# Kernel optimization log

Measured on AMD Instinct MI355X. Metric: run time of the kernel, lower is better.

## Reference

```python
import jax, jax.numpy as jnp
import numpy as np

WIN = 7          # gaussian window size (odd)
SIGMA = 1.5
DOWNSCALE = 2
C1 = 0.01 ** 2
C2 = 0.03 ** 2


def _gauss_window(dtype):
    x = jnp.arange(WIN, dtype=jnp.float32) - (WIN - 1) / 2
    g = jnp.exp(-x ** 2 / (2 * SIGMA ** 2))
    g = g / g.sum()
    w2d = jnp.outer(g, g)                      # (7,7)
    return w2d[None, None].astype(dtype)       # OIHW = (1,1,7,7)


def _avg_pool(x, k):
    if k == 1:
        return x
    s = jax.lax.reduce_window(x, 0.0, jax.lax.add,
                              (1, 1, k, k), (1, 1, k, k), 'VALID')
    return s / (k * k)


def _blur(x, w):
    pad = WIN // 2
    return jax.lax.conv_general_dilated(
        x, w, window_strides=(1, 1),
        padding=[(pad, pad), (pad, pad)],
        dimension_numbers=('NCHW', 'OIHW', 'NCHW'))


def setup_inputs() -> dict:
    key = jax.random.key(0)
    k1, k2 = jax.random.split(key)
    shape = (16, 1, 768, 1024)
    pred = jax.random.uniform(k1, shape, dtype=jnp.float32)
    target = jax.random.uniform(k2, shape, dtype=jnp.float32)
    return {"pred": pred, "target": target}


def reference(pred, target):
    p = _avg_pool(pred, DOWNSCALE)
    t = _avg_pool(target, DOWNSCALE)
    w = _gauss_window(p.dtype)

    mu1 = _blur(p, w)
    mu2 = _blur(t, w)
    mu1_sq = mu1 * mu1
    mu2_sq = mu2 * mu2
    mu1_mu2 = mu1 * mu2

    sigma1_sq = _blur(p * p, w) - mu1_sq
    sigma2_sq = _blur(t * t, w) - mu2_sq
    sigma12 = _blur(p * t, w) - mu1_mu2

    num = (2 * mu1_mu2 + C1) * (2 * sigma12 + C2)
    den = (mu1_sq + mu2_sq + C1) * (sigma1_sq + sigma2_sq + C2)
    ssim_map = num / (den + 1e-12)
    return 1.0 - ssim_map.mean()
```

## Files before the change

kernel.cpp:

```cpp
#include <hip/hip_runtime.h>
#include <math.h>

#define NIMG 16
#define IH 768
#define IW 1024
#define HD 384
#define WD 512
#define TH 16
#define TW 64
#define HALO 3
#define RH (TH + 2*HALO)
#define RW (TW + 2*HALO)
#define RWP 72
#define NGX (WD/TW)
#define NGY (HD/TH)
#define NBLK (NGX*NGY*NIMG)
#define SSIM_C1 1.0e-4f
#define SSIM_C2 9.0e-4f

struct GW { float g[7]; };

__global__ __launch_bounds__(256, 4) void ssim_main(
    const float* __restrict__ pred, const float* __restrict__ tgt,
    float* __restrict__ partial, GW gw)
{
  __shared__ float p_s[RH][RWP];
  __shared__ float t_s[RH][RWP];
  __shared__ float vb[5][TH][RWP];
  __shared__ float wred[4];

  const int tid = threadIdx.x;
  const int bx = blockIdx.x, by = blockIdx.y, n = blockIdx.z;
  const int tx0 = bx * TW, ty0 = by * TH;
  const float* __restrict__ pb = pred + (size_t)n * IH * IW;
  const float* __restrict__ tb = tgt  + (size_t)n * IH * IW;

  for (int idx = tid; idx < RH * RW; idx += 256) {
    const int ly = idx / RW;
    const int lx = idx - ly * RW;
    const int gy = ty0 + ly - HALO;
    const int gx = tx0 + lx - HALO;
    float pv = 0.f, tv = 0.f;
    if ((unsigned)gy < (unsigned)HD && (unsigned)gx < (unsigned)WD) {
      const size_t o0 = (size_t)(2 * gy) * IW + (size_t)(2 * gx);
      const float2 a = *(const float2*)(pb + o0);
      const float2 b = *(const float2*)(pb + o0 + IW);
      const float2 c = *(const float2*)(tb + o0);
      const float2 d = *(const float2*)(tb + o0 + IW);
      pv = 0.25f * ((a.x + a.y) + (b.x + b.y));
      tv = 0.25f * ((c.x + c.y) + (d.x + d.y));
    }
    p_s[ly][lx] = pv;
    t_s[ly][lx] = tv;
  }
  __syncthreads();

  for (int idx = tid; idx < TH * (RWP/4); idx += 256) {
    const int y  = idx / (RWP/4);
    const int c4 = (idx - y * (RWP/4)) * 4;
    float m1_0=0,m1_1=0,m1_2=0,m1_3=0;
    float m2_0=0,m2_1=0,m2_2=0,m2_3=0;
    float pp_0=0,pp_1=0,pp_2=0,pp_3=0;
    float tt_0=0,tt_1=0,tt_2=0,tt_3=0;
    float pt_0=0,pt_1=0,pt_2=0,pt_3=0;
#pragma unroll
    for (int k = 0; k < 7; ++k) {
      const float w = gw.g[k];
      const float4 P = *(const float4*)&p_s[y + k][c4];
      const float4 T = *(const float4*)&t_s[y + k][c4];
      m1_0 += w*P.x;        m1_1 += w*P.y;        m1_2 += w*P.z;        m1_3 += w*P.w;
      m2_0 += w*T.x;        m2_1 += w*T.y;        m2_2 += w*T.z;        m2_3 += w*T.w;
      pp_0 += w*(P.x*P.x);  pp_1 += w*(P.y*P.y);  pp_2 += w*(P.z*P.z);  pp_3 += w*(P.w*P.w);
      tt_0 += w*(T.x*T.x);  tt_1 += w*(T.y*T.y);  tt_2 += w*(T.z*T.z);  tt_3 += w*(T.w*T.w);
      pt_0 += w*(P.x*T.x);  pt_1 += w*(P.y*T.y);  pt_2 += w*(P.z*T.z);  pt_3 += w*(P.w*T.w);
    }
    *(float4*)&vb[0][y][c4] = make_float4(m1_0, m1_1, m1_2, m1_3);
    *(float4*)&vb[1][y][c4] = make_float4(m2_0, m2_1, m2_2, m2_3);
    *(float4*)&vb[2][y][c4] = make_float4(pp_0, pp_1, pp_2, pp_3);
    *(float4*)&vb[3][y][c4] = make_float4(tt_0, tt_1, tt_2, tt_3);
    *(float4*)&vb[4][y][c4] = make_float4(pt_0, pt_1, pt_2, pt_3);
  }
  __syncthreads();

  float lsum = 0.f;
  for (int idx = tid; idx < TH * (TW/4); idx += 256) {
    const int y  = idx / (TW/4);
    const int c0 = (idx - y * (TW/4)) * 4;
    float w0[12], w1[12], w2[12], w3[12], w4[12];
#define LDCH(arr, ch) { \
      const float4 A = *(const float4*)&vb[ch][y][c0];     \
      const float4 B = *(const float4*)&vb[ch][y][c0 + 4]; \
      const float4 C = *(const float4*)&vb[ch][y][c0 + 8]; \
      arr[0]=A.x; arr[1]=A.y; arr[2]=A.z;  arr[3]=A.w;     \
      arr[4]=B.x; arr[5]=B.y; arr[6]=B.z;  arr[7]=B.w;     \
      arr[8]=C.x; arr[9]=C.y; arr[10]=C.z; arr[11]=C.w; }
    LDCH(w0, 0) LDCH(w1, 1) LDCH(w2, 2) LDCH(w3, 3) LDCH(w4, 4)
#undef LDCH
#pragma unroll
    for (int j = 0; j < 4; ++j) {
      float mu1 = 0.f, mu2 = 0.f, bpp = 0.f, btt = 0.f, bpt = 0.f;
#pragma unroll
      for (int k = 0; k < 7; ++k) {
        const float w = gw.g[k];
        mu1 += w * w0[j + k];
        mu2 += w * w1[j + k];
        bpp += w * w2[j + k];
        btt += w * w3[j + k];
        bpt += w * w4[j + k];
      }
      const float mu1sq = mu1 * mu1;
      const float mu2sq = mu2 * mu2;
      const float mu12  = mu1 * mu2;
      const float s1    = bpp - mu1sq;
      const float s2    = btt - mu2sq;
      const float s12   = bpt - mu12;
      const float num = (2.f * mu12 + SSIM_C1) * (2.f * s12 + SSIM_C2);
      const float den = (mu1sq + mu2sq + SSIM_C1) * (s1 + s2 + SSIM_C2);
      lsum += num / (den + 1e-12f);
    }
  }

#pragma unroll
  for (int off = 32; off > 0; off >>= 1)
    lsum += __shfl_down(lsum, off, 64);
  if ((tid & 63) == 0) wred[tid >> 6] = lsum;
  __syncthreads();
  if (tid == 0)
    partial[((size_t)n * NGY + by) * NGX + bx] =
        wred[0] + wred[1] + wred[2] + wred[3];
}

__global__ __launch_bounds__(256) void ssim_final(
    const float* __restrict__ partial, float* __restrict__ out)
{
  __shared__ float red[4];
  float s = 0.f;
  for (int i = threadIdx.x; i < NBLK; i += 256) s += partial[i];
#pragma unroll
  for (int off = 32; off > 0; off >>= 1)
    s += __shfl_down(s, off, 64);
  if ((threadIdx.x & 63) == 0) red[threadIdx.x >> 6] = s;
  __syncthreads();
  if (threadIdx.x == 0) {
    const float tot = red[0] + red[1] + red[2] + red[3];
    out[0] = 1.0f - tot * (1.0f / (float)((size_t)NIMG * HD * WD));
  }
}

extern "C" void kernel_launch(void* const* d_in, const int* in_sizes, int n_in,
                              void* d_out, int out_size, void* d_ws, size_t ws_size,
                              hipStream_t stream) {
  const float* pred = (const float*)d_in[0];
  const float* tgt  = (const float*)d_in[1];
  float* out     = (float*)d_out;
  float* partial = (float*)d_ws;

  GW gw;
  double gd[7], s = 0.0;
  for (int i = 0; i < 7; ++i) {
    const double x = (double)i - 3.0;
    gd[i] = exp(-x * x / (2.0 * 1.5 * 1.5));
    s += gd[i];
  }
  for (int i = 0; i < 7; ++i) gw.g[i] = (float)(gd[i] / s);

  dim3 grid(NGX, NGY, NIMG);
  ssim_main<<<grid, 256, 0, stream>>>(pred, tgt, partial, gw);
  ssim_final<<<1, 256, 0, stream>>>(partial, out);
}
```

Baseline: 139.8 us.

## Fuse vertical and horizontal blur passes in registers, vectorize halo loads

Removes the shared-memory intermediate buffer holding the five vertical-blur channels and its barrier. Each thread now computes vertical sums for 12 columns in registers and then applies the horizontal blur directly. The horizontal halo widens to 4 so global loads can be float4, with two downsampled pixels per slot. Occupancy hint is raised to 5 waves. The cost is about three times more vertical-blur arithmetic per thread, because neighbouring threads recompute overlapping columns, plus higher register pressure.

```diff
diff --git a/kernel.cpp b/kernel.cpp
--- a/kernel.cpp
+++ b/kernel.cpp
@@ -8,10 +8,12 @@
 #define WD 512
 #define TH 16
 #define TW 64
-#define HALO 3
-#define RH (TH + 2*HALO)
-#define RW (TW + 2*HALO)
-#define RWP 72
+#define HALO_Y 3
+#define HALO_X 4
+#define RH (TH + 2*HALO_Y)
+#define RW (TW + 2*HALO_X)
+#define NPAIR (RW/2)
+#define NSLOT (RH*NPAIR)
 #define NGX (WD/TW)
 #define NGY (HD/TH)
 #define NBLK (NGX*NGY*NIMG)
@@ -20,13 +22,12 @@
 
 struct GW { float g[7]; };
 
-__global__ __launch_bounds__(256, 4) void ssim_main(
+__global__ __launch_bounds__(256, 5) void ssim_main(
     const float* __restrict__ pred, const float* __restrict__ tgt,
     float* __restrict__ partial, GW gw)
 {
-  __shared__ float p_s[RH][RWP];
-  __shared__ float t_s[RH][RWP];
-  __shared__ float vb[5][TH][RWP];
+  __shared__ float p_s[RH][RW];
+  __shared__ float t_s[RH][RW];
   __shared__ float wred[4];
 
   const int tid = threadIdx.x;
@@ -35,89 +36,83 @@
   const float* __restrict__ pb = pred + (size_t)n * IH * IW;
   const float* __restrict__ tb = tgt  + (size_t)n * IH * IW;
 
-  for (int idx = tid; idx < RH * RW; idx += 256) {
-    const int ly = idx / RW;
-    const int lx = idx - ly * RW;
-    const int gy = ty0 + ly - HALO;
-    const int gx = tx0 + lx - HALO;
-    float pv = 0.f, tv = 0.f;
-    if ((unsigned)gy < (unsigned)HD && (unsigned)gx < (unsigned)WD) {
-      const size_t o0 = (size_t)(2 * gy) * IW + (size_t)(2 * gx);
-      const float2 a = *(const float2*)(pb + o0);
-      const float2 b = *(const float2*)(pb + o0 + IW);
-      const float2 c = *(const float2*)(tb + o0);
-      const float2 d = *(const float2*)(tb + o0 + IW);
-      pv = 0.25f * ((a.x + a.y) + (b.x + b.y));
-      tv = 0.25f * ((c.x + c.y) + (d.x + d.y));
+#pragma unroll
+  for (int i = 0; i < 4; ++i) {
+    const int slot = tid + i * 256;
+    if (slot < NSLOT) {
+      const int row  = slot / NPAIR;
+      const int pair = slot - row * NPAIR;
+      const int gy = ty0 + row - HALO_Y;
+      const int pg = tx0 + 2 * pair - HALO_X;
+      float pv0 = 0.f, pv1 = 0.f, tv0 = 0.f, tv1 = 0.f;
+      if ((unsigned)gy < (unsigned)HD && (unsigned)pg < (unsigned)WD) {
+        const size_t o0 = (size_t)(2 * gy) * IW + (size_t)(2 * pg);
+        const float4 a = *(const float4*)(pb + o0);
+        const float4 b = *(const float4*)(pb + o0 + IW);
+        const float4 c = *(const float4*)(tb + o0);
+        const float4 d = *(const float4*)(tb + o0 + IW);
+        pv0 = 0.25f * ((a.x + a.y) + (b.x + b.y));
+        pv1 = 0.25f * ((a.z + a.w) + (b.z + b.w));
+        tv0 = 0.25f * ((c.x + c.y) + (d.x + d.y));
+        tv1 = 0.25f * ((c.z + c.w) + (d.z + d.w));
+      }
+      *(float2*)&p_s[row][2 * pair] = make_float2(pv0, pv1);
+      *(float2*)&t_s[row][2 * pair] = make_float2(tv0, tv1);
     }
-    p_s[ly][lx] = pv;
-    t_s[ly][lx] = tv;
   }
   __syncthreads();
 
-  for (int idx = tid; idx < TH * (RWP/4); idx += 256) {
-    const int y  = idx / (RWP/4);
-    const int c4 = (idx - y * (RWP/4)) * 4;
-    float m1_0=0,m1_1=0,m1_2=0,m1_3=0;
-    float m2_0=0,m2_1=0,m2_2=0,m2_3=0;
-    float pp_0=0,pp_1=0,pp_2=0,pp_3=0;
-    float tt_0=0,tt_1=0,tt_2=0,tt_3=0;
-    float pt_0=0,pt_1=0,pt_2=0,pt_3=0;
+  const int y  = tid >> 4;
+  const int c0 = (tid & 15) << 2;
+
+  float a1[12], a2[12], app[12], att[12], apt[12];
+#pragma unroll
+  for (int i = 0; i < 12; ++i) { a1[i]=0.f; a2[i]=0.f; app[i]=0.f; att[i]=0.f; apt[i]=0.f; }
+
+#pragma unroll
+  for (int k = 0; k < 7; ++k) {
+    const float w = gw.g[k];
+#pragma unroll
+    for (int g = 0; g < 3; ++g) {
+      const float4 P = *(const float4*)&p_s[y + k][c0 + 4 * g];
+      const float4 T = *(const float4*)&t_s[y + k][c0 + 4 * g];
+      const int b = 4 * g;
+      a1[b+0] = fmaf(w, P.x, a1[b+0]);  a1[b+1] = fmaf(w, P.y, a1[b+1]);
+      a1[b+2] = fmaf(w, P.z, a1[b+2]);  a1[b+3] = fmaf(w, P.w, a1[b+3]);
+      a2[b+0] = fmaf(w, T.x, a2[b+0]);  a2[b+1] = fmaf(w, T.y, a2[b+1]);
+      a2[b+2] = fmaf(w, T.z, a2[b+2]);  a2[b+3] = fmaf(w, T.w, a2[b+3]);
+      app[b+0] = fmaf(w, P.x*P.x, app[b+0]);  app[b+1] = fmaf(w, P.y*P.y, app[b+1]);
+      app[b+2] = fmaf(w, P.z*P.z, app[b+2]);  app[b+3] = fmaf(w, P.w*P.w, app[b+3]);
+      att[b+0] = fmaf(w, T.x*T.x, att[b+0]);  att[b+1] = fmaf(w, T.y*T.y, att[b+1]);
+      att[b+2] = fmaf(w, T.z*T.z, att[b+2]);  att[b+3] = fmaf(w, T.w*T.w, att[b+3]);
+      apt[b+0] = fmaf(w, P.x*T.x, apt[b+0]);  apt[b+1] = fmaf(w, P.y*T.y, apt[b+1]);
+      apt[b+2] = fmaf(w, P.z*T.z, apt[b+2]);  apt[b+3] = fmaf(w, P.w*T.w, apt[b+3]);
+    }
+  }
+
+  float lsum = 0.f;
+#pragma unroll
+  for (int j = 0; j < 4; ++j) {
+    float mu1 = 0.f, mu2 = 0.f, bpp = 0.f, btt = 0.f, bpt = 0.f;
 #pragma unroll
     for (int k = 0; k < 7; ++k) {
       const float w = gw.g[k];
-      const float4 P = *(const float4*)&p_s[y + k][c4];
-      const float4 T = *(const float4*)&t_s[y + k][c4];
-      m1_0 += w*P.x;        m1_1 += w*P.y;        m1_2 += w*P.z;        m1_3 += w*P.w;
-      m2_0 += w*T.x;        m2_1 += w*T.y;        m2_2 += w*T.z;        m2_3 += w*T.w;
-      pp_0 += w*(P.x*P.x);  pp_1 += w*(P.y*P.y);  pp_2 += w*(P.z*P.z);  pp_3 += w*(P.w*P.w);
-      tt_0 += w*(T.x*T.x);  tt_1 += w*(T.y*T.y);  tt_2 += w*(T.z*T.z);  tt_3 += w*(T.w*T.w);
-      pt_0 += w*(P.x*T.x);  pt_1 += w*(P.y*T.y);  pt_2 += w*(P.z*T.z);  pt_3 += w*(P.w*T.w);
+      const int idx = j + 1 + k;
+      mu1 = fmaf(w, a1[idx],  mu1);
+      mu2 = fmaf(w, a2[idx],  mu2);
+      bpp = fmaf(w, app[idx], bpp);
+      btt = fmaf(w, att[idx], btt);
+      bpt = fmaf(w, apt[idx], bpt);
     }
-    *(float4*)&vb[0][y][c4] = make_float4(m1_0, m1_1, m1_2, m1_3);
-    *(float4*)&vb[1][y][c4] = make_float4(m2_0, m2_1, m2_2, m2_3);
-    *(float4*)&vb[2][y][c4] = make_float4(pp_0, pp_1, pp_2, pp_3);
-    *(float4*)&vb[3][y][c4] = make_float4(tt_0, tt_1, tt_2, tt_3);
-    *(float4*)&vb[4][y][c4] = make_float4(pt_0, pt_1, pt_2, pt_3);
-  }
-  __syncthreads();
-
-  float lsum = 0.f;
-  for (int idx = tid; idx < TH * (TW/4); idx += 256) {
-    const int y  = idx / (TW/4);
-    const int c0 = (idx - y * (TW/4)) * 4;
-    float w0[12], w1[12], w2[12], w3[12], w4[12];
-#define LDCH(arr, ch) { \
-      const float4 A = *(const float4*)&vb[ch][y][c0];     \
-      const float4 B = *(const float4*)&vb[ch][y][c0 + 4]; \
-      const float4 C = *(const float4*)&vb[ch][y][c0 + 8]; \
-      arr[0]=A.x; arr[1]=A.y; arr[2]=A.z;  arr[3]=A.w;     \
-      arr[4]=B.x; arr[5]=B.y; arr[6]=B.z;  arr[7]=B.w;     \
-      arr[8]=C.x; arr[9]=C.y; arr[10]=C.z; arr[11]=C.w; }
-    LDCH(w0, 0) LDCH(w1, 1) LDCH(w2, 2) LDCH(w3, 3) LDCH(w4, 4)
-#undef LDCH
-#pragma unroll
-    for (int j = 0; j < 4; ++j) {
-      float mu1 = 0.f, mu2 = 0.f, bpp = 0.f, btt = 0.f, bpt = 0.f;
-#pragma unroll
-      for (int k = 0; k < 7; ++k) {
-        const float w = gw.g[k];
-        mu1 += w * w0[j + k];
-        mu2 += w * w1[j + k];
-        bpp += w * w2[j + k];
-        btt += w * w3[j + k];
-        bpt += w * w4[j + k];
-      }
-      const float mu1sq = mu1 * mu1;
-      const float mu2sq = mu2 * mu2;
-      const float mu12  = mu1 * mu2;
-      const float s1    = bpp - mu1sq;
-      const float s2    = btt - mu2sq;
-      const float s12   = bpt - mu12;
-      const float num = (2.f * mu12 + SSIM_C1) * (2.f * s12 + SSIM_C2);
-      const float den = (mu1sq + mu2sq + SSIM_C1) * (s1 + s2 + SSIM_C2);
-      lsum += num / (den + 1e-12f);
-    }
+    const float mu1sq = mu1 * mu1;
+    const float mu2sq = mu2 * mu2;
+    const float mu12  = mu1 * mu2;
+    const float s1    = bpp - mu1sq;
+    const float s2    = btt - mu2sq;
+    const float s12   = bpt - mu12;
+    const float num = (2.f * mu12 + SSIM_C1) * (2.f * s12 + SSIM_C2);
+    const float den = (mu1sq + mu2sq + SSIM_C1) * (s1 + s2 + SSIM_C2);
+    lsum += num / (den + 1e-12f);
   }
 
 #pragma unroll
```

Result: faster. 134.2 us (-4.0%).
